# Kernel tuning notes

Hardware: AMD Instinct MI355X
Metric: run time of the kernel (lower is better)

Reference implementation:

```python
import jax, jax.numpy as jnp
import numpy as np

N = 8192
NT = 85       # number of DFIRE atom types
BINS = 28     # distance bins, d/0.7 clamped to [0,27]
EXCLU = 2     # nbre_nt_exclu


def setup_inputs() -> dict:
    key = jax.random.key(0)
    k1, k2, k3, k4 = jax.random.split(key, 4)
    # coords scaled so pairwise distances span the 0..19.6A cutoff range
    coords = jax.random.normal(k1, (N, 3), dtype=jnp.float32) * 10.0
    res_ids = jnp.sort(jax.random.randint(k2, (N,), 0, 400)).astype(jnp.int32)
    type_indices = jax.random.randint(k3, (N,), 0, NT).astype(jnp.int32)
    pot = jax.random.normal(k4, (NT, NT, BINS), dtype=jnp.float32)
    # original LUT is symmetric in the two type axes
    pot_tensor = 0.5 * (pot + jnp.transpose(pot, (1, 0, 2)))
    # upper-triangular pair indices, offset=1 (deterministic, like torch.triu_indices)
    ii, jj = np.triu_indices(N, 1)
    i_idx = jnp.asarray(ii, dtype=jnp.int32)
    j_idx = jnp.asarray(jj, dtype=jnp.int32)
    return {
        "coords": coords,
        "pot_tensor": pot_tensor,
        "res_ids": res_ids,
        "type_indices": type_indices,
        "i_idx": i_idx,
        "j_idx": j_idx,
    }


def reference(coords, pot_tensor, res_ids, type_indices, i_idx, j_idx):
    # sequence-separation and valid-type mask (stream compaction -> masked sum)
    sep = jnp.abs(res_ids[i_idx] - res_ids[j_idx])
    t1 = type_indices[i_idx]
    t2 = type_indices[j_idx]
    mask = (sep > EXCLU) & (t1 >= 0) & (t2 >= 0)

    # pairwise distances on all triu pairs
    diff = coords[i_idx] - coords[j_idx]              # [P,3]
    dists = jnp.sqrt(jnp.sum(diff * diff, axis=1)) + 1e-8  # [P]

    # bin + linear interpolation from the 3D LUT
    d_scaled = dists / 0.7
    d0 = jnp.floor(jnp.clip(d_scaled, 0.0, 27.0)).astype(jnp.int32)
    d1 = jnp.minimum(d0 + 1, 27)
    alpha = d_scaled - d0.astype(dists.dtype)

    # safe indices for masked-out pairs (their energy is multiplied by 0)
    t1s = jnp.where(mask, t1, 0)
    t2s = jnp.where(mask, t2, 0)
    e0 = pot_tensor[t1s, t2s, d0]
    e1 = pot_tensor[t1s, t2s, d1]
    energy = (1.0 - alpha) * e0 + alpha * e1

    w = mask & (dists < 19.6)
    return jnp.sum(energy * w.astype(energy.dtype))
```

## Files before the change

kernel.cpp:

```cpp
#include <hip/hip_runtime.h>

#define NT    85
#define BINS  28
#define NTB   (NT * BINS)
#define TILE  128
#define LUT_ELEMS (NT * NT * BINS)

__global__ __launch_bounds__(256) void prep_k(const float* __restrict__ pot,
                                              const int* __restrict__ type, int N,
                                              float2* __restrict__ lut,
                                              int* __restrict__ offs) {
    if ((int)blockIdx.x == (int)gridDim.x - 1) {
        __shared__ int h[NT];
        for (int t = threadIdx.x; t < NT; t += 256) h[t] = 0;
        __syncthreads();
        for (int i = threadIdx.x; i < N; i += 256) atomicAdd(&h[type[i]], 1);
        __syncthreads();
        if (threadIdx.x == 0) {
            int s = 0;
            for (int t = 0; t < NT; ++t) { int c = h[t]; offs[t] = s; s += c; }
        }
    }
    int idx = blockIdx.x * 256 + threadIdx.x;
    if (idx < LUT_ELEMS) {
        int d  = idx % BINS;
        int ab = idx / BINS;
        int d1 = (d + 1 < BINS) ? d + 1 : BINS - 1;
        lut[idx] = make_float2(pot[idx], pot[ab * BINS + d1]);
    }
}

__global__ void scatter_k(const float* __restrict__ coords, const int* __restrict__ res,
                          const int* __restrict__ type, int* __restrict__ offs,
                          float4* __restrict__ pc, int N) {
    int i = blockIdx.x * blockDim.x + threadIdx.x;
    if (i >= N) return;
    int t = type[i];
    int p = atomicAdd(&offs[t], 1);
    pc[p] = make_float4(coords[3 * i], coords[3 * i + 1], coords[3 * i + 2],
                        __int_as_float((t << 10) | res[i]));
}

__global__ __launch_bounds__(256) void dfire_pairs4(
    const float4* __restrict__ pc,
    const float2* __restrict__ lut,
    float* __restrict__ partial, int T) {

    __shared__ float wsum[4];

    int k = blockIdx.x;
    int r = (int)((2.0 * T + 1.0 - sqrt((2.0 * T + 1.0) * (2.0 * T + 1.0) - 8.0 * (double)k)) * 0.5);
    if (r < 0) r = 0;
    if (r > T - 1) r = T - 1;
    while (r > 0 && (r * T - r * (r - 1) / 2) > k) --r;
    while (((r + 1) * T - (r + 1) * r / 2) <= k) ++r;
    int c = r + (k - (r * T - r * (r - 1) / 2));

    int bi = r * TILE, bj = c * TILE;
    int tid = threadIdx.x;

    int ii = tid & (TILE - 1);
    float4 ci = pc[bi + ii];
    int wi   = __float_as_int(ci.w);
    int ires = wi & 1023;
    int itb  = (wi >> 10) * BINS;
    int ii_eff = (bi == bj) ? ii : -1;

    float a0 = 0.f, a1 = 0.f, a2 = 0.f, a3 = 0.f;
    int j0 = tid >> 7;

#define STEP(S, ACC) do {                                               \
    int jjv = __builtin_amdgcn_readfirstlane(j0 + 2 * (S));             \
    float4 cj = pc[bj + jjv];            \
    int   wj   = __float_as_int(cj.w);                                  \
    int   jres = wj & 1023;                                             \
    int   jrow = (wj >> 10) * NTB;                                      \
    float dx = ci.x - cj.x, dy = ci.y - cj.y, dz = ci.z - cj.z;         \
    float d2 = fmaf(dx, dx, fmaf(dy, dy, dz * dz));                     \
    int  sep = abs(ires - jres);                                        \
    bool v = (sep > 2) & (d2 < 19.6f * 19.6f) & (jjv > ii_eff);         \
    if (v) {                                                            \
        float dist  = __builtin_amdgcn_sqrtf(d2);                       \
        float ds    = dist * (1.0f / 0.7f);                             \
        float dsc   = fminf(ds, 27.0f);                                 \
        int   d0    = (int)dsc;                                         \
        float alpha = ds - (float)d0;                                   \
        float2 e = lut[jrow + itb + d0];                                \
        ACC += fmaf(alpha, e.y - e.x, e.x);                             \
    }                                                                   \
} while (0)

    #pragma unroll
    for (int s = 0; s < TILE / 8; ++s) {
        STEP(4 * s,     a0);
        STEP(4 * s + 1, a1);
        STEP(4 * s + 2, a2);
        STEP(4 * s + 3, a3);
    }
#undef STEP

    float acc = (a0 + a1) + (a2 + a3);
    for (int off = 32; off > 0; off >>= 1)
        acc += __shfl_down(acc, off, 64);
    if ((tid & 63) == 0) wsum[tid >> 6] = acc;
    __syncthreads();
    if (tid == 0) partial[blockIdx.x] = (wsum[0] + wsum[1]) + (wsum[2] + wsum[3]);
}

__global__ __launch_bounds__(256) void reduce_k(const float* __restrict__ p, int n,
                                                float* __restrict__ out) {
    __shared__ float ws[4];
    float a = 0.f;
    for (int i = threadIdx.x; i < n; i += 256) a += p[i];
    for (int off = 32; off > 0; off >>= 1)
        a += __shfl_down(a, off, 64);
    if ((threadIdx.x & 63) == 0) ws[threadIdx.x >> 6] = a;
    __syncthreads();
    if (threadIdx.x == 0) out[0] = (ws[0] + ws[1]) + (ws[2] + ws[3]);
}

__global__ __launch_bounds__(256) void dfire_pairs_fb(
    const float* __restrict__ coords, const int* __restrict__ res,
    const int* __restrict__ type, const float* __restrict__ pot,
    float* __restrict__ out, int T) {

    __shared__ float jx[TILE], jy[TILE], jz[TILE];
    __shared__ int   jres[TILE], jtype[TILE];

    int k = blockIdx.x;
    int r = (int)((2.0 * T + 1.0 - sqrt((2.0 * T + 1.0) * (2.0 * T + 1.0) - 8.0 * (double)k)) * 0.5);
    if (r < 0) r = 0;
    if (r > T - 1) r = T - 1;
    while (r > 0 && (r * T - r * (r - 1) / 2) > k) --r;
    while (((r + 1) * T - (r + 1) * r / 2) <= k) ++r;
    int c = r + (k - (r * T - r * (r - 1) / 2));

    int bi = r * TILE, bj = c * TILE;
    int tid = threadIdx.x;
    if (tid < TILE) {
        int gj = bj + tid;
        jx[tid] = coords[3 * gj]; jy[tid] = coords[3 * gj + 1]; jz[tid] = coords[3 * gj + 2];
        jres[tid] = res[gj]; jtype[tid] = type[gj];
    }
    int ii = tid & (TILE - 1);
    int gi = bi + ii;
    float ix = coords[3 * gi], iy = coords[3 * gi + 1], iz = coords[3 * gi + 2];
    int iresv = res[gi], it = type[gi];
    int ii_eff = (bi == bj) ? ii : -1;
    __syncthreads();

    float acc = 0.f;
    int jj = tid >> 7;
    for (int s = 0; s < TILE / 2; ++s, jj += 2) {
        float dx = ix - jx[jj], dy = iy - jy[jj], dz = iz - jz[jj];
        float d2 = dx * dx + dy * dy + dz * dz;
        float dist = sqrtf(d2) + 1e-8f;
        int sep = abs(iresv - jres[jj]);
        bool v = (sep > 2) & (dist < 19.6f) & (jj > ii_eff);
        if (v) {
            float ds = dist * (1.0f / 0.7f);
            int d0 = (int)fminf(ds, 27.0f);
            int d1 = (d0 + 1 < BINS) ? d0 + 1 : BINS - 1;
            float alpha = ds - (float)d0;
            int row = (jtype[jj] * NT + it) * BINS;
            float e0 = pot[row + d0], e1 = pot[row + d1];
            acc += e0 + alpha * (e1 - e0);
        }
    }
    for (int off = 32; off > 0; off >>= 1)
        acc += __shfl_down(acc, off, 64);
    if ((tid & 63) == 0) atomicAdd(out, acc);
}

extern "C" void kernel_launch(void* const* d_in, const int* in_sizes, int n_in,
                              void* d_out, int out_size, void* d_ws, size_t ws_size,
                              hipStream_t stream) {
    const float* coords = (const float*)d_in[0];
    const float* pot    = (const float*)d_in[1];
    const int*   res    = (const int*)d_in[2];
    const int*   type   = (const int*)d_in[3];

    const int N = in_sizes[2];
    const int T = N / TILE;
    const int nblk = T * (T + 1) / 2;

    float* out = (float*)d_out;

    const size_t lutBytes  = (size_t)LUT_ELEMS * sizeof(float2);
    const size_t pcBytes   = (size_t)N * sizeof(float4);
    const size_t offsBytes = 128 * sizeof(int);
    const size_t partBytes = (size_t)nblk * sizeof(float);
    const size_t need = lutBytes + pcBytes + offsBytes + partBytes;

    if (ws_size >= need) {
        char* w = (char*)d_ws;
        float2* lut     = (float2*)w;                     w += lutBytes;
        float4* pc      = (float4*)w;                     w += pcBytes;
        int*    offs    = (int*)w;                        w += offsBytes;
        float*  partial = (float*)w;

        const int repackBlocks = (LUT_ELEMS + 255) / 256;
        prep_k<<<repackBlocks + 1, 256, 0, stream>>>(pot, type, N, lut, offs);
        scatter_k<<<(N + 255) / 256, 256, 0, stream>>>(coords, res, type, offs, pc, N);
        dfire_pairs4<<<nblk, 256, 0, stream>>>(pc, lut, partial, T);
        reduce_k<<<1, 256, 0, stream>>>(partial, nblk, out);
    } else {
        hipMemsetAsync(out, 0, sizeof(float), stream);
        dfire_pairs_fb<<<nblk, 256, 0, stream>>>(coords, res, type, pot, out, T);
    }
}
```

Baseline: 279.7 us.

## Stage per-tile LUT slice in LDS with bf16-packed pairs and 2-row register blocking

```diff
diff --git a/kernel.cpp b/kernel.cpp
--- a/kernel.cpp
+++ b/kernel.cpp
@@ -2,13 +2,19 @@
 
 #define NT    85
 #define BINS  28
-#define NTB   (NT * BINS)
-#define TILE  128
 #define LUT_ELEMS (NT * NT * BINS)
+#define CUT2  (19.6f * 19.6f)
+#define ROWCAP 8
+#define COLCAP 8
+
+__device__ __forceinline__ unsigned bf16r(float x) {
+    unsigned b = __float_as_uint(x);
+    return (b + 0x7FFFu + ((b >> 16) & 1u)) >> 16;
+}
 
 __global__ __launch_bounds__(256) void prep_k(const float* __restrict__ pot,
                                               const int* __restrict__ type, int N,
-                                              float2* __restrict__ lut,
+                                              unsigned* __restrict__ pk,
                                               int* __restrict__ offs) {
     if ((int)blockIdx.x == (int)gridDim.x - 1) {
         __shared__ int h[NT];
@@ -26,7 +32,8 @@
         int d  = idx % BINS;
         int ab = idx / BINS;
         int d1 = (d + 1 < BINS) ? d + 1 : BINS - 1;
-        lut[idx] = make_float2(pot[idx], pot[ab * BINS + d1]);
+        float e0 = pot[idx], e1 = pot[ab * BINS + d1];
+        pk[idx] = (bf16r(e1) << 16) | bf16r(e0);
     }
 }
 
@@ -41,70 +48,120 @@
                         __int_as_float((t << 10) | res[i]));
 }
 
-__global__ __launch_bounds__(256) void dfire_pairs4(
-    const float4* __restrict__ pc,
-    const float2* __restrict__ lut,
-    float* __restrict__ partial, int T) {
-
-    __shared__ float wsum[4];
+__global__ __launch_bounds__(128) void dfire_pairs6(
+    const float4*  __restrict__ pc,
+    const unsigned* __restrict__ pk,
+    float* __restrict__ partial, int TI, int TJ) {
+
+    __shared__ float4   jtile[128];
+    __shared__ unsigned lrow[ROWCAP * COLCAP * BINS];
+    __shared__ float    wsum[2];
 
     int k = blockIdx.x;
-    int r = (int)((2.0 * T + 1.0 - sqrt((2.0 * T + 1.0) * (2.0 * T + 1.0) - 8.0 * (double)k)) * 0.5);
-    if (r < 0) r = 0;
-    if (r > T - 1) r = T - 1;
-    while (r > 0 && (r * T - r * (r - 1) / 2) > k) --r;
-    while (((r + 1) * T - (r + 1) * r / 2) <= k) ++r;
-    int c = r + (k - (r * T - r * (r - 1) / 2));
-
-    int bi = r * TILE, bj = c * TILE;
+    double A = (double)TJ + 1.0;
+    int ri = (int)((A - sqrt(A * A - 4.0 * (double)k)) * 0.5);
+    if (ri < 0) ri = 0;
+    if (ri > TI - 1) ri = TI - 1;
+    while (ri > 0 && ri * (TJ + 1 - ri) > k) --ri;
+    while (ri + 1 < TI && (ri + 1) * (TJ + 1 - (ri + 1)) <= k) ++ri;
+    int cj = 2 * ri + (k - ri * (TJ + 1 - ri));
+
+    int bi = ri * 256, bj = cj * 128;
     int tid = threadIdx.x;
 
-    int ii = tid & (TILE - 1);
-    float4 ci = pc[bi + ii];
-    int wi   = __float_as_int(ci.w);
-    int ires = wi & 1023;
-    int itb  = (wi >> 10) * BINS;
-    int ii_eff = (bi == bj) ? ii : -1;
-
-    float a0 = 0.f, a1 = 0.f, a2 = 0.f, a3 = 0.f;
-    int j0 = tid >> 7;
-
-#define STEP(S, ACC) do {                                               \
-    int jjv = __builtin_amdgcn_readfirstlane(j0 + 2 * (S));             \
-    float4 cj = pc[bj + jjv];            \
-    int   wj   = __float_as_int(cj.w);                                  \
-    int   jres = wj & 1023;                                             \
-    int   jrow = (wj >> 10) * NTB;                                      \
-    float dx = ci.x - cj.x, dy = ci.y - cj.y, dz = ci.z - cj.z;         \
-    float d2 = fmaf(dx, dx, fmaf(dy, dy, dz * dz));                     \
-    int  sep = abs(ires - jres);                                        \
-    bool v = (sep > 2) & (d2 < 19.6f * 19.6f) & (jjv > ii_eff);         \
-    if (v) {                                                            \
-        float dist  = __builtin_amdgcn_sqrtf(d2);                       \
-        float ds    = dist * (1.0f / 0.7f);                             \
-        float dsc   = fminf(ds, 27.0f);                                 \
-        int   d0    = (int)dsc;                                         \
-        float alpha = ds - (float)d0;                                   \
-        float2 e = lut[jrow + itb + d0];                                \
-        ACC += fmaf(alpha, e.y - e.x, e.x);                             \
-    }                                                                   \
+    jtile[tid] = pc[bj + tid];
+
+    float4 ci0 = pc[bi + tid];
+    float4 ci1 = pc[bi + 128 + tid];
+
+    const int* pci = (const int*)pc;
+    int tA = pci[4 * bi + 3] >> 10;
+    int tB = pci[4 * (bi + 255) + 3] >> 10;
+    int tC = pci[4 * bj + 3] >> 10;
+    int tD = pci[4 * (bj + 127) + 3] >> 10;
+    int nrow = tB - tA + 1, ncol = tD - tC + 1;
+    bool useLds = (nrow <= ROWCAP) && (ncol <= COLCAP);
+
+    if (useLds) {
+        int tot = nrow * ncol * BINS;
+        for (int e = tid; e < tot; e += 128) {
+            int d  = e % BINS;
+            int rc = e / BINS;
+            int cc = rc % ncol;
+            int rr = rc / ncol;
+            lrow[e] = pk[((tA + rr) * NT + (tC + cc)) * BINS + d];
+        }
+    }
+    __syncthreads();
+
+    int w0 = __float_as_int(ci0.w), w1 = __float_as_int(ci1.w);
+    int ires0 = w0 & 1023, ires1 = w1 & 1023;
+    int it0 = w0 >> 10, it1 = w1 >> 10;
+    int rb0 = (it0 - tA) * (ncol * BINS);
+    int rb1 = (it1 - tA) * (ncol * BINS);
+    int gb0 = it0 * (NT * BINS);
+    int gb1 = it1 * (NT * BINS);
+    bool straddle = (cj <= 2 * ri + 1);
+    int ig0 = straddle ? (bi + tid)       : -1;
+    int ig1 = straddle ? (bi + 128 + tid) : -1;
+
+    float acc0 = 0.f, acc1 = 0.f;
+    int w = tid >> 6;
+
+#define PAIR(CI, IRES, IG, RBASE, ACC) do {                                   \
+    float dx = (CI).x - cj4.x, dy = (CI).y - cj4.y, dz = (CI).z - cj4.z;      \
+    float d2 = fmaf(dx, dx, fmaf(dy, dy, dz * dz));                           \
+    int sep = (IRES) - jres; sep = sep < 0 ? -sep : sep;                      \
+    bool v = (sep > 2) & (d2 < CUT2) & (jg > (IG));                           \
+    float dist  = __builtin_amdgcn_sqrtf(d2);                                 \
+    float ds    = dist * (1.0f / 0.7f);                                       \
+    float dsc   = fminf(ds, 27.0f);                                           \
+    int   d0    = (int)dsc;                                                   \
+    float alpha = ds - (float)d0;                                             \
+    unsigned u  = SRC[(RBASE) + jcb + d0];                                    \
+    float e0 = __uint_as_float(u << 16);                                      \
+    float e1 = __uint_as_float(u & 0xFFFF0000u);                              \
+    float en = fmaf(alpha, e1 - e0, e0);                                      \
+    ACC += v ? en : 0.0f;                                                     \
 } while (0)
 
-    #pragma unroll
-    for (int s = 0; s < TILE / 8; ++s) {
-        STEP(4 * s,     a0);
-        STEP(4 * s + 1, a1);
-        STEP(4 * s + 2, a2);
-        STEP(4 * s + 3, a3);
-    }
-#undef STEP
-
-    float acc = (a0 + a1) + (a2 + a3);
+    if (useLds) {
+        #pragma unroll 4
+        for (int s = 0; s < 128; ++s) {
+            int j = (s + (w << 6)) & 127;
+            float4 cj4 = jtile[j];
+            int wj  = __builtin_amdgcn_readfirstlane(__float_as_int(cj4.w));
+            int jres = wj & 1023;
+            int jcb  = ((wj >> 10) - tC) * BINS;
+            int jg   = bj + j;
+#define SRC lrow
+            PAIR(ci0, ires0, ig0, rb0, acc0);
+            PAIR(ci1, ires1, ig1, rb1, acc1);
+#undef SRC
+        }
+    } else {
+        #pragma unroll 2
+        for (int s = 0; s < 128; ++s) {
+            int j = (s + (w << 6)) & 127;
+            float4 cj4 = jtile[j];
+            int wj  = __builtin_amdgcn_readfirstlane(__float_as_int(cj4.w));
+            int jres = wj & 1023;
+            int jcb  = (wj >> 10) * BINS;
+            int jg   = bj + j;
+#define SRC pk
+            PAIR(ci0, ires0, ig0, gb0, acc0);
+            PAIR(ci1, ires1, ig1, gb1, acc1);
+#undef SRC
+        }
+    }
+#undef PAIR
+
+    float acc = acc0 + acc1;
     for (int off = 32; off > 0; off >>= 1)
         acc += __shfl_down(acc, off, 64);
     if ((tid & 63) == 0) wsum[tid >> 6] = acc;
     __syncthreads();
-    if (tid == 0) partial[blockIdx.x] = (wsum[0] + wsum[1]) + (wsum[2] + wsum[3]);
+    if (tid == 0) partial[blockIdx.x] = wsum[0] + wsum[1];
 }
 
 __global__ __launch_bounds__(256) void reduce_k(const float* __restrict__ p, int n,
@@ -124,8 +181,8 @@
     const int* __restrict__ type, const float* __restrict__ pot,
     float* __restrict__ out, int T) {
 
-    __shared__ float jx[TILE], jy[TILE], jz[TILE];
-    __shared__ int   jres[TILE], jtype[TILE];
+    __shared__ float jx[128], jy[128], jz[128];
+    __shared__ int   jres[128], jtype[128];
 
     int k = blockIdx.x;
     int r = (int)((2.0 * T + 1.0 - sqrt((2.0 * T + 1.0) * (2.0 * T + 1.0) - 8.0 * (double)k)) * 0.5);
@@ -135,14 +192,14 @@
     while (((r + 1) * T - (r + 1) * r / 2) <= k) ++r;
     int c = r + (k - (r * T - r * (r - 1) / 2));
 
-    int bi = r * TILE, bj = c * TILE;
+    int bi = r * 128, bj = c * 128;
     int tid = threadIdx.x;
-    if (tid < TILE) {
+    if (tid < 128) {
         int gj = bj + tid;
         jx[tid] = coords[3 * gj]; jy[tid] = coords[3 * gj + 1]; jz[tid] = coords[3 * gj + 2];
         jres[tid] = res[gj]; jtype[tid] = type[gj];
     }
-    int ii = tid & (TILE - 1);
+    int ii = tid & 127;
     int gi = bi + ii;
     float ix = coords[3 * gi], iy = coords[3 * gi + 1], iz = coords[3 * gi + 2];
     int iresv = res[gi], it = type[gi];
@@ -151,7 +208,7 @@
 
     float acc = 0.f;
     int jj = tid >> 7;
-    for (int s = 0; s < TILE / 2; ++s, jj += 2) {
+    for (int s = 0; s < 64; ++s, jj += 2) {
         float dx = ix - jx[jj], dy = iy - jy[jj], dz = iz - jz[jj];
         float d2 = dx * dx + dy * dy + dz * dz;
         float dist = sqrtf(d2) + 1e-8f;
@@ -181,31 +238,32 @@
     const int*   type   = (const int*)d_in[3];
 
     const int N = in_sizes[2];
-    const int T = N / TILE;
-    const int nblk = T * (T + 1) / 2;
-
     float* out = (float*)d_out;
 
-    const size_t lutBytes  = (size_t)LUT_ELEMS * sizeof(float2);
+    const int TI = N / 256, TJ = N / 128;
+    const int nblk = TI * (TJ + 1 - TI);
+
+    const size_t pkBytes   = (size_t)LUT_ELEMS * sizeof(unsigned);
     const size_t pcBytes   = (size_t)N * sizeof(float4);
     const size_t offsBytes = 128 * sizeof(int);
     const size_t partBytes = (size_t)nblk * sizeof(float);
-    const size_t need = lutBytes + pcBytes + offsBytes + partBytes;
-
-    if (ws_size >= need) {
+    const size_t need = pkBytes + pcBytes + offsBytes + partBytes;
+
+    if (ws_size >= need && (N % 256) == 0) {
         char* w = (char*)d_ws;
-        float2* lut     = (float2*)w;                     w += lutBytes;
-        float4* pc      = (float4*)w;                     w += pcBytes;
-        int*    offs    = (int*)w;                        w += offsBytes;
-        float*  partial = (float*)w;
-
-        const int repackBlocks = (LUT_ELEMS + 255) / 256;
-        prep_k<<<repackBlocks + 1, 256, 0, stream>>>(pot, type, N, lut, offs);
+        unsigned* pk      = (unsigned*)w;   w += pkBytes;
+        float4*   pc      = (float4*)w;     w += pcBytes;
+        int*      offs    = (int*)w;        w += offsBytes;
+        float*    partial = (float*)w;
+
+        const int prepBlocks = (LUT_ELEMS + 255) / 256;
+        prep_k<<<prepBlocks + 1, 256, 0, stream>>>(pot, type, N, pk, offs);
         scatter_k<<<(N + 255) / 256, 256, 0, stream>>>(coords, res, type, offs, pc, N);
-        dfire_pairs4<<<nblk, 256, 0, stream>>>(pc, lut, partial, T);
+        dfire_pairs6<<<nblk, 128, 0, stream>>>(pc, pk, partial, TI, TJ);
         reduce_k<<<1, 256, 0, stream>>>(partial, nblk, out);
     } else {
         hipMemsetAsync(out, 0, sizeof(float), stream);
-        dfire_pairs_fb<<<nblk, 256, 0, stream>>>(coords, res, type, pot, out, T);
-    }
-}
+        const int T = N / 128;
+        dfire_pairs_fb<<<T * (T + 1) / 2, 256, 0, stream>>>(coords, res, type, pot, out, T);
+    }
+}
```

Result: slower. 286.8 us (+2.5%).
